# Optimization experiments

Hardware: AMD Instinct MI355X
Metric: run time of the kernel (lower is better)

Reference implementation:

```python
import jax, jax.numpy as jnp
import numpy as np

BN_EPS = 1e-5
STRIDE = 2


def setup_inputs() -> dict:
    key = jax.random.key(0)
    ks = jax.random.split(key, 8)
    B, T, Cin = 32, 1024, 128
    F, K, H = 256, 5, 512
    return {
        "x": jax.random.normal(ks[0], (B, T, Cin), jnp.float32),
        "conv_w": jax.random.normal(ks[1], (F, Cin, K), jnp.float32) * 0.05,
        "conv_b": jax.random.normal(ks[2], (F,), jnp.float32) * 0.05,
        "bn_gamma": jnp.ones((F,), jnp.float32),
        "bn_beta": jnp.zeros((F,), jnp.float32),
        "bn_mean": jnp.zeros((F,), jnp.float32),
        "bn_var": jnp.ones((F,), jnp.float32),
        "w_ih": jax.random.normal(ks[3], (4 * H, F), jnp.float32) * 0.04,
        "w_hh": jax.random.normal(ks[4], (4 * H, H), jnp.float32) * 0.04,
        "b_ih": jnp.zeros((4 * H,), jnp.float32),
        "b_hh": jnp.zeros((4 * H,), jnp.float32),
        "w_uh": jax.random.normal(ks[5], (1, H), jnp.float32) * 0.04,
        "b_uh": jnp.ones((1,), jnp.float32),
    }


def _skip_lstm(xs, w_ih, w_hh, b_ih, b_hh, w_uh, b_uh):
    # xs: [B, T', F] conv features. Skip-LSTM cell (Campos et al. Skip RNN):
    # standard LSTM + binarized state-update gate u with straight-through estimator.
    B, Tc, Fdim = xs.shape
    H = w_hh.shape[1]
    h0 = jnp.zeros((B, H), xs.dtype)
    c0 = jnp.zeros((B, H), xs.dtype)
    u0 = jnp.ones((B, 1), xs.dtype)
    # precompute input contribution to gates: [T', B, 4H]
    x_proj = jnp.einsum('btf,gf->tbg', xs, w_ih) + b_ih + b_hh

    def step(carry, xp):
        h, c, u = carry
        gates = xp + h @ w_hh.T
        i, f, g, o = jnp.split(gates, 4, axis=-1)
        c_t = jax.nn.sigmoid(f) * c + jax.nn.sigmoid(i) * jnp.tanh(g)
        h_t = jax.nn.sigmoid(o) * jnp.tanh(c_t)
        # straight-through binarization of update probability
        u_bin = u + jax.lax.stop_gradient(jnp.round(u) - u)
        c_new = u_bin * c_t + (1.0 - u_bin) * c
        h_new = u_bin * h_t + (1.0 - u_bin) * h
        du = jax.nn.sigmoid(c_new @ w_uh.T + b_uh)
        u_new = u_bin * du + (1.0 - u_bin) * (u + jnp.minimum(du, 1.0 - u))
        return (h_new, c_new, u_new), h_new

    _, hs = jax.lax.scan(step, (h0, c0, u0), x_proj)
    return jnp.swapaxes(hs, 0, 1)  # [B, T', H]


def reference(x, conv_w, conv_b, bn_gamma, bn_beta, bn_mean, bn_var,
              w_ih, w_hh, b_ih, b_hh, w_uh, b_uh):
    # Conv1d + ReLU + BatchNorm1d (eval-mode stats) on [B, Cin, T]
    xc = jnp.swapaxes(x, 1, 2)
    y = jax.lax.conv_general_dilated(
        xc, conv_w, (STRIDE,), 'VALID',
        dimension_numbers=('NCH', 'OIH', 'NCH'))
    y = jax.nn.relu(y + conv_b[None, :, None])
    inv = bn_gamma / jnp.sqrt(bn_var + BN_EPS)
    y = y * inv[None, :, None] + (bn_beta - bn_mean * inv)[None, :, None]
    y = jnp.swapaxes(y, 1, 2)  # [B, T', F]
    hs = _skip_lstm(y, w_ih, w_hh, b_ih, b_hh, w_uh, b_uh)
    return hs[:, -1, :]
```

## Files before the change

### kernel.cpp

```cpp
#include <hip/hip_runtime.h>
#include <stdint.h>
#include <math.h>

#define BB 32
#define TT 1024
#define CIN 128
#define FF 256
#define KW 5
#define HH 512
#define TP 510
#define TLAST 509
#define KC 640
#define GWG 256

#define HPK_OFF     0ull
#define PRT_OFF     262144ull
#define XP_OFF      278528ull
#define XH_OFF      (XP_OFF + 134217728ull)
#define XL_OFF      (XH_OFF + 8388608ull)
#define XSH_OFF     (XL_OFF + 8388608ull)
#define XSL_OFF     (XSH_OFF + 8388608ull)
#define WCH_OFF     (XSL_OFF + 8388608ull)
#define WCL_OFF     (WCH_OFF + 327680ull)
#define WIHH_OFF    (WCL_OFF + 327680ull)
#define WIHL_OFF    (WIHH_OFF + 1048576ull)
#define WS_NEED     (WIHL_OFF + 1048576ull)

typedef unsigned short u16;
typedef unsigned long long u64;
typedef __attribute__((ext_vector_type(8))) short short8;
typedef __attribute__((ext_vector_type(4))) float f32x4;
typedef __attribute__((ext_vector_type(4))) unsigned int u32x4;

__device__ __forceinline__ u16 f2bf(float f) {
  uint32_t u = __float_as_uint(f);
  u += 0x7fffu + ((u >> 16) & 1u);
  return (u16)(u >> 16);
}
__device__ __forceinline__ float bf2f(u16 s) { return __uint_as_float(((uint32_t)s) << 16); }
__device__ __forceinline__ void splitf(float v, u16& h, u16& l) {
  h = f2bf(v);
  l = f2bf(v - bf2f(h));
}
__device__ __forceinline__ float sigm(float x) {
  return __fdividef(1.f, 1.f + __expf(-x));
}
__device__ __forceinline__ float tanh_fast(float x) {
  float xc = fminf(x, 20.f);
  float e = __expf(2.f * xc);
  return (e - 1.f) * __fdividef(1.f, e + 1.f);
}

__global__ void prep_kernel(const float* __restrict__ x, const float* __restrict__ conv_w,
                            const float* __restrict__ w_ih,
                            u16* __restrict__ xh, u16* __restrict__ xl,
                            u16* __restrict__ wch, u16* __restrict__ wcl,
                            u16* __restrict__ wihh, u16* __restrict__ wihl) {
  int i = blockIdx.x * 256 + threadIdx.x;
  if (i < 4194304) {
    u16 h, l; splitf(x[i], h, l); xh[i] = h; xl[i] = l;
  } else if (i < 4194304 + 163840) {
    int j = i - 4194304;
    int f = j / 640, kk = j % 640;
    int c = kk & 127, k = kk >> 7;
    u16 h, l; splitf(conv_w[f * 640 + c * 5 + k], h, l);
    wch[f * 640 + kk] = h; wcl[f * 640 + kk] = l;
  } else if (i < 4194304 + 163840 + 524288) {
    int j = i - (4194304 + 163840);
    u16 h, l; splitf(w_ih[j], h, l); wihh[j] = h; wihl[j] = l;
  }
}

template <int MODE>
__global__ __launch_bounds__(256, 1) void gemm_kernel(
    const u16* __restrict__ Ah, const u16* __restrict__ Al,
    const u16* __restrict__ Bh, const u16* __restrict__ Bl,
    const float* __restrict__ e0, const float* __restrict__ e1,
    const float* __restrict__ e2, const float* __restrict__ e3, const float* __restrict__ e4,
    u16* __restrict__ outh, u16* __restrict__ outl, float* __restrict__ outf) {
  const int KDIM = (MODE == 0) ? KC : 256;
  const int MT   = (MODE == 0) ? 2 : 16;
  int bx = blockIdx.x;
  int m0 = (bx % MT) * 128;
  int n0 = (bx / MT) * 128;
  __shared__ __attribute__((aligned(16))) u16 lds[4][4096];
  int t = threadIdx.x;
  int wave = t >> 6, lane = t & 63;
  int wm = wave & 1, wn = wave >> 1;

  f32x4 acc[4][4];
#pragma unroll
  for (int i = 0; i < 4; i++)
#pragma unroll
    for (int j = 0; j < 4; j++) acc[i][j] = (f32x4){0.f, 0.f, 0.f, 0.f};

  for (int k0 = 0; k0 < KDIM; k0 += 32) {
    __syncthreads();
#pragma unroll
    for (int half = 0; half < 2; half++) {
      int e = half * 256 + t;
      int l = e & 63, tile = e >> 6;
      int kk = k0 + ((l >> 4) * 8);
      {
        int row = m0 + tile * 16 + (l & 15);
        const u16* sh = Ah + (long)row * KDIM + kk;
        const u16* sl = Al + (long)row * KDIM + kk;
        *(short8*)&lds[0][e * 8] = *(const short8*)sh;
        *(short8*)&lds[1][e * 8] = *(const short8*)sl;
      }
      {
        int n = n0 + tile * 16 + (l & 15);
        long base;
        if (MODE == 0) {
          int tp = n >> 5; if (tp > TLAST) tp = TLAST;
          base = (long)(n & 31) * 131072 + (long)tp * 256;
        } else {
          base = (long)n * 256;
        }
        *(short8*)&lds[2][e * 8] = *(const short8*)(Bh + base + kk);
        *(short8*)&lds[3][e * 8] = *(const short8*)(Bl + base + kk);
      }
    }
    __syncthreads();
    short8 af[4][2], bf[4][2];
#pragma unroll
    for (int i = 0; i < 4; i++) {
      af[i][0] = *(const short8*)&lds[0][((wm * 4 + i) * 64 + lane) * 8];
      af[i][1] = *(const short8*)&lds[1][((wm * 4 + i) * 64 + lane) * 8];
      bf[i][0] = *(const short8*)&lds[2][((wn * 4 + i) * 64 + lane) * 8];
      bf[i][1] = *(const short8*)&lds[3][((wn * 4 + i) * 64 + lane) * 8];
    }
#pragma unroll
    for (int am = 0; am < 4; am++)
#pragma unroll
      for (int an = 0; an < 4; an++) {
        acc[am][an] = __builtin_amdgcn_mfma_f32_16x16x32_bf16(af[am][0], bf[an][0], acc[am][an], 0, 0, 0);
        acc[am][an] = __builtin_amdgcn_mfma_f32_16x16x32_bf16(af[am][0], bf[an][1], acc[am][an], 0, 0, 0);
        acc[am][an] = __builtin_amdgcn_mfma_f32_16x16x32_bf16(af[am][1], bf[an][0], acc[am][an], 0, 0, 0);
      }
  }
#pragma unroll
  for (int am = 0; am < 4; am++)
#pragma unroll
    for (int an = 0; an < 4; an++) {
      int n = n0 + (wn * 4 + an) * 16 + (lane & 15);
#pragma unroll
      for (int r = 0; r < 4; r++) {
        int m = m0 + (wm * 4 + am) * 16 + (lane >> 4) * 4 + r;
        float v = acc[am][an][r];
        if (MODE == 0) {
          float inv = e1[m] / sqrtf(e4[m] + 1e-5f);
          float sh  = e2[m] - e3[m] * inv;
          v = fmaxf(v + e0[m], 0.f) * inv + sh;
          u16 h, l; splitf(v, h, l);
          outh[(long)n * 256 + m] = h;
          outl[(long)n * 256 + m] = l;
        } else {
          v += e0[m] + e1[m];
          int tp = n >> 5, b = n & 31;
          int grp = b >> 2, bb = b & 3;
          int q = m >> 9, unit = m & 511;
          int sl = unit >> 4, jjj = unit & 15;
          outf[(((long)grp * 512 + tp) * 32 + sl) * 256 + q * 64 + jjj * 4 + bb] = v;
        }
      }
    }
}

__global__ __launch_bounds__(256, 1) void scan_kernel(
    const float* __restrict__ xpg,
    const float* __restrict__ w_hh,
    const float* __restrict__ w_uh,
    const float* __restrict__ b_uh_p,
    uint32_t* __restrict__ hpk,
    u64* __restrict__ prt,
    float* __restrict__ outp)
{
  __shared__ __attribute__((aligned(16))) u16 sh_hi[4 * 528];
  __shared__ __attribute__((aligned(16))) u16 sh_lo[4 * 528];
  __shared__ float gpart[4][4][16][5];
  __shared__ float sparts[4][32];
  __shared__ int   arrive_l[32];
  __shared__ float u_l[4], ubin_l[4];
  __shared__ float wuh_l[16];
  int group = blockIdx.x & 7, slot = blockIdx.x >> 3;
  int t = threadIdx.x;
  int wave = t >> 6, lane = t & 63;
  int um = lane & 15, kq = lane >> 4;
  int nbc = um & 3;

  if (t < 16) wuh_l[t] = w_uh[slot * 16 + t];
  if (t < 4)  { u_l[t] = 1.0f; ubin_l[t] = 1.0f; }
  if (t < 32) arrive_l[t] = 0;

  short8 wfh[4][4], wfl[4][4];
#pragma unroll
  for (int q = 0; q < 4; q++) {
    long row = (long)(q * 512 + slot * 16 + um) * 512;
#pragma unroll
    for (int k4 = 0; k4 < 4; k4++) {
      union { short8 v; u16 u[8]; } Uh, Ul;
      long col0 = wave * 128 + k4 * 32 + kq * 8;
#pragma unroll
      for (int i = 0; i < 8; i++) splitf(w_hh[row + col0 + i], Uh.u[i], Ul.u[i]);
      wfh[q][k4] = Uh.v; wfl[q][k4] = Ul.v;
    }
  }
  float bu = b_uh_p[0];

  bool cell = (lane < 16);
  int  cb = wave, cj = lane;
  float c_reg = 0.f, h_reg = 0.f;

  uint32_t* hgrp = hpk + (long)group * 4096;
  u64*      pgrp = prt + (long)group * 256;

  __syncthreads();

  for (int s = 0; s < TP; s++) {
    int par = s & 1, np = par ^ 1;
    f32x4 xq;
    if (cell) {
      const float* xb = xpg + (((long)group * 512 + s) * 32 + slot) * 256;
      float x0 = xb[0 * 64 + cj * 4 + cb];
      float x1 = xb[1 * 64 + cj * 4 + cb];
      float x2 = xb[2 * 64 + cj * 4 + cb];
      float x3 = xb[3 * 64 + cj * 4 + cb];
      xq = (f32x4){x0, x1, x2, x3};
    }
    int b = t >> 6, u0 = (t & 63) * 8;
    if (s == 0) {
      *(u32x4*)&sh_hi[b * 528 + u0] = (u32x4){0u, 0u, 0u, 0u};
      *(u32x4*)&sh_lo[b * 528 + u0] = (u32x4){0u, 0u, 0u, 0u};
    } else {
      int pslot = (t & 63) >> 1;
      const u64* pw = pgrp + (long)par * 128 + b * 32 + pslot;
      const u64* hp = (const u64*)(hgrp + (long)par * 2048 + b * 512 + u0);
      uint32_t tg = (uint32_t)s;
      uint32_t e = (((uint32_t)(s - 1) >> 1) & 1u) ^ 1u;
      bool needp = ((t & 1) == 0);
      u64 v0 = __hip_atomic_load(hp,     __ATOMIC_RELAXED, __HIP_MEMORY_SCOPE_AGENT);
      u64 v1 = __hip_atomic_load(hp + 1, __ATOMIC_RELAXED, __HIP_MEMORY_SCOPE_AGENT);
      u64 v2 = __hip_atomic_load(hp + 2, __ATOMIC_RELAXED, __HIP_MEMORY_SCOPE_AGENT);
      u64 v3 = __hip_atomic_load(hp + 3, __ATOMIC_RELAXED, __HIP_MEMORY_SCOPE_AGENT);
      u64 w0 = 0;
      if (b == 0 || needp)
        w0 = __hip_atomic_load(pw, __ATOMIC_RELAXED, __HIP_MEMORY_SCOPE_AGENT);
      if (b == 0) {
        u64 w = w0;
        while ((uint32_t)(w >> 32) != tg)
          w = __hip_atomic_load(pw, __ATOMIC_RELAXED, __HIP_MEMORY_SCOPE_AGENT);
        if (needp) {
          sparts[0][pslot] = __uint_as_float((uint32_t)w);
          ((volatile int*)arrive_l)[pslot] = s;
        }
      } else {
        volatile int* arr = (volatile int*)&arrive_l[pslot];
        while (*arr != s) {}
        if (needp) {
          u64 w = w0;
          while ((uint32_t)(w >> 32) != tg)
            w = __hip_atomic_load(pw, __ATOMIC_RELAXED, __HIP_MEMORY_SCOPE_AGENT);
          sparts[b][pslot] = __uint_as_float((uint32_t)w);
        }
      }
      for (;;) {
        uint32_t bad = (((uint32_t)v0 ^ e) | ((uint32_t)(v0 >> 32) ^ e) |
                        ((uint32_t)v1 ^ e) | ((uint32_t)(v1 >> 32) ^ e) |
                        ((uint32_t)v2 ^ e) | ((uint32_t)(v2 >> 32) ^ e) |
                        ((uint32_t)v3 ^ e) | ((uint32_t)(v3 >> 32) ^ e)) & 1u;
        if (!bad) break;
        v0 = __hip_atomic_load(hp,     __ATOMIC_RELAXED, __HIP_MEMORY_SCOPE_AGENT);
        v1 = __hip_atomic_load(hp + 1, __ATOMIC_RELAXED, __HIP_MEMORY_SCOPE_AGENT);
        v2 = __hip_atomic_load(hp + 2, __ATOMIC_RELAXED, __HIP_MEMORY_SCOPE_AGENT);
        v3 = __hip_atomic_load(hp + 3, __ATOMIC_RELAXED, __HIP_MEMORY_SCOPE_AGENT);
      }
      uint32_t p[8] = {(uint32_t)v0, (uint32_t)(v0 >> 32), (uint32_t)v1, (uint32_t)(v1 >> 32),
                       (uint32_t)v2, (uint32_t)(v2 >> 32), (uint32_t)v3, (uint32_t)(v3 >> 32)};
      u32x4 hv, lv;
#pragma unroll
      for (int r = 0; r < 4; r++) {
        hv[r] = __builtin_amdgcn_perm(p[2 * r + 1], p[2 * r], 0x07060302u);
        lv[r] = __builtin_amdgcn_perm(p[2 * r + 1], p[2 * r], 0x05040100u);
      }
      *(u32x4*)&sh_hi[b * 528 + u0] = hv;
      *(u32x4*)&sh_lo[b * 528 + u0] = lv;
    }
    __syncthreads();
    if (s > 0 && t < 4) {
      float a = 0.f;
#pragma unroll
      for (int i = 0; i < 32; i++) a += sparts[t][i];
      float du = sigm(a + bu);
      float up = u_l[t], ubp = ubin_l[t];
      float un = (ubp > 0.5f) ? du : (up + fminf(du, 1.f - up));
      u_l[t] = un; ubin_l[t] = rintf(un);
    }
    f32x4 A0[4], A1[4], A2[4];
#pragma unroll
    for (int q = 0; q < 4; q++) {
      A0[q] = (f32x4){0.f, 0.f, 0.f, 0.f}; A1[q] = A0[q]; A2[q] = A0[q];
    }
#pragma unroll
    for (int k4 = 0; k4 < 4; k4++) {
      int ko = (wave * 4 + k4) * 32 + kq * 8;
      short8 bh = *(const short8*)&sh_hi[nbc * 528 + ko];
      short8 bl = *(const short8*)&sh_lo[nbc * 528 + ko];
#pragma unroll
      for (int q = 0; q < 4; q++) {
        A0[q] = __builtin_amdgcn_mfma_f32_16x16x32_bf16(wfh[q][k4], bh, A0[q], 0, 0, 0);
        A1[q] = __builtin_amdgcn_mfma_f32_16x16x32_bf16(wfh[q][k4], bl, A1[q], 0, 0, 0);
        A2[q] = __builtin_amdgcn_mfma_f32_16x16x32_bf16(wfl[q][k4], bh, A2[q], 0, 0, 0);
      }
    }
    if (um < 4) {
#pragma unroll
      for (int q = 0; q < 4; q++)
#pragma unroll
        for (int r = 0; r < 4; r++)
          gpart[wave][q][kq * 4 + r][um] = (A0[q][r] + A1[q][r]) + A2[q][r];
    }
    __syncthreads();
    if (cell) {
      float g[4];
#pragma unroll
      for (int q = 0; q < 4; q++) {
        float a = xq[q];
#pragma unroll
        for (int w = 0; w < 4; w++) a += gpart[w][q][cj][cb];
        g[q] = a;
      }
      float ig = sigm(g[0]), fg = sigm(g[1]), og = sigm(g[3]);
      float gt = tanh_fast(g[2]);
      float ct = fg * c_reg + ig * gt;
      float ht = og * tanh_fast(ct);
      bool upd = ubin_l[cb] > 0.5f;
      float cn = upd ? ct : c_reg;
      float hn = upd ? ht : h_reg;
      c_reg = cn; h_reg = hn;
      u16 hhi, hlo; splitf(hn, hhi, hlo);
      uint32_t mk = (((uint32_t)s >> 1) & 1u) ^ 1u;
      hlo = (u16)((hlo & 0xFFFEu) | mk);
      uint32_t pk = ((uint32_t)hhi << 16) | (uint32_t)hlo;
      __hip_atomic_store(hgrp + (long)np * 2048 + cb * 512 + slot * 16 + cj, pk,
                         __ATOMIC_RELAXED, __HIP_MEMORY_SCOPE_AGENT);
      float pr = cn * wuh_l[cj];
      pr += __shfl_xor(pr, 1); pr += __shfl_xor(pr, 2);
      pr += __shfl_xor(pr, 4); pr += __shfl_xor(pr, 8);
      if (s == TLAST) outp[(long)(group * 4 + cb) * 512 + slot * 16 + cj] = hn;
      if (cj == 0) {
        u64 pw = ((u64)(uint32_t)(s + 1) << 32) | (u64)__float_as_uint(pr);
        __hip_atomic_store(pgrp + (long)np * 128 + cb * 32 + slot, pw,
                           __ATOMIC_RELAXED, __HIP_MEMORY_SCOPE_AGENT);
      }
    }
  }
}

extern "C" void kernel_launch(void* const* d_in, const int* in_sizes, int n_in,
                              void* d_out, int out_size, void* d_ws, size_t ws_size,
                              hipStream_t stream) {
  const float* x      = (const float*)d_in[0];
  const float* conv_w = (const float*)d_in[1];
  const float* conv_b = (const float*)d_in[2];
  const float* gamma  = (const float*)d_in[3];
  const float* beta   = (const float*)d_in[4];
  const float* mean   = (const float*)d_in[5];
  const float* var    = (const float*)d_in[6];
  const float* w_ih   = (const float*)d_in[7];
  const float* w_hh   = (const float*)d_in[8];
  const float* b_ih   = (const float*)d_in[9];
  const float* b_hh   = (const float*)d_in[10];
  const float* w_uh   = (const float*)d_in[11];
  const float* b_uh   = (const float*)d_in[12];
  float* out = (float*)d_out;

  if (ws_size < WS_NEED) return;

  char* w = (char*)d_ws;
  uint32_t* hpk = (uint32_t*)(w + HPK_OFF);
  u64*   prt   = (u64*)(w + PRT_OFF);
  float* xp    = (float*)(w + XP_OFF);
  u16*   xh    = (u16*)(w + XH_OFF);
  u16*   xl    = (u16*)(w + XL_OFF);
  u16*   xsh   = (u16*)(w + XSH_OFF);
  u16*   xsl   = (u16*)(w + XSL_OFF);
  u16*   wch   = (u16*)(w + WCH_OFF);
  u16*   wcl   = (u16*)(w + WCL_OFF);
  u16*   wihh  = (u16*)(w + WIHH_OFF);
  u16*   wihl  = (u16*)(w + WIHL_OFF);


  prep_kernel<<<19072, 256, 0, stream>>>(x, conv_w, w_ih, xh, xl, wch, wcl, wihh, wihl);

  gemm_kernel<0><<<2 * 128, 256, 0, stream>>>(wch, wcl, xh, xl,
                                              conv_b, gamma, beta, mean, var,
                                              xsh, xsl, nullptr);
  gemm_kernel<1><<<16 * 128, 256, 0, stream>>>(wihh, wihl, xsh, xsl,
                                               b_ih, b_hh, nullptr, nullptr, nullptr,
                                               nullptr, nullptr, xp);
  scan_kernel<<<GWG, 256, 0, stream>>>(xp, w_hh, w_uh, b_uh, hpk, prt, out);
}
```

Before: 1.725 ms.

## Regroup scan into 2 groups of 16 batch rows to fill MFMA columns

The recurrent scan now splits the 32 batch rows into 2 groups of 16 instead of 8 groups of 4, cutting the workgroup count from 256 to 64. Each workgroup now fills all 16 MFMA N columns with distinct batch rows rather than replicating 4, and every lane performs a cell update. The x-projection output layout and the inter-workgroup flag and partial-sum buffers are resized to match. This removes wasted MFMA columns and idle lanes, but each step now moves more h data per workgroup and fewer CUs share the work.

```diff
diff --git a/kernel.cpp b/kernel.cpp
--- a/kernel.cpp
+++ b/kernel.cpp
@@ -11,7 +11,7 @@
 #define TP 510
 #define TLAST 509
 #define KC 640
-#define GWG 256
+#define GWG 64
 
 #define HPK_OFF     0ull
 #define PRT_OFF     262144ull
@@ -31,6 +31,8 @@
 typedef __attribute__((ext_vector_type(8))) short short8;
 typedef __attribute__((ext_vector_type(4))) float f32x4;
 typedef __attribute__((ext_vector_type(4))) unsigned int u32x4;
+
+#define AL(p) __hip_atomic_load((p), __ATOMIC_RELAXED, __HIP_MEMORY_SCOPE_AGENT)
 
 __device__ __forceinline__ u16 f2bf(float f) {
   uint32_t u = __float_as_uint(f);
@@ -158,10 +160,10 @@
         } else {
           v += e0[m] + e1[m];
           int tp = n >> 5, b = n & 31;
-          int grp = b >> 2, bb = b & 3;
+          int grp = b >> 4, bb = b & 15;
           int q = m >> 9, unit = m & 511;
           int sl = unit >> 4, jjj = unit & 15;
-          outf[(((long)grp * 512 + tp) * 32 + sl) * 256 + q * 64 + jjj * 4 + bb] = v;
+          outf[((((long)grp * 512 + tp) * 32 + sl) * 4 + q) * 256 + bb * 16 + jjj] = v;
         }
       }
     }
@@ -176,21 +178,20 @@
     u64* __restrict__ prt,
     float* __restrict__ outp)
 {
-  __shared__ __attribute__((aligned(16))) u16 sh_hi[4 * 528];
-  __shared__ __attribute__((aligned(16))) u16 sh_lo[4 * 528];
-  __shared__ float gpart[4][4][16][5];
-  __shared__ float sparts[4][32];
+  __shared__ __attribute__((aligned(16))) u16 sh_hi[16 * 528];
+  __shared__ __attribute__((aligned(16))) u16 sh_lo[16 * 528];
+  __shared__ float gpart[4][4][16][17];
+  __shared__ float sparts[16][32];
   __shared__ int   arrive_l[32];
-  __shared__ float u_l[4], ubin_l[4];
+  __shared__ float u_l[16], ubin_l[16];
   __shared__ float wuh_l[16];
-  int group = blockIdx.x & 7, slot = blockIdx.x >> 3;
+  int group = blockIdx.x & 1, slot = blockIdx.x >> 1;
   int t = threadIdx.x;
   int wave = t >> 6, lane = t & 63;
   int um = lane & 15, kq = lane >> 4;
-  int nbc = um & 3;
 
   if (t < 16) wuh_l[t] = w_uh[slot * 16 + t];
-  if (t < 4)  { u_l[t] = 1.0f; ubin_l[t] = 1.0f; }
+  if (t < 16) { u_l[t] = 1.0f; ubin_l[t] = 1.0f; }
   if (t < 32) arrive_l[t] = 0;
 
   short8 wfh[4][4], wfl[4][4];
@@ -208,86 +209,92 @@
   }
   float bu = b_uh_p[0];
 
-  bool cell = (lane < 16);
-  int  cb = wave, cj = lane;
+  int cb = wave * 4 + kq, cj = um;
   float c_reg = 0.f, h_reg = 0.f;
 
-  uint32_t* hgrp = hpk + (long)group * 4096;
-  u64*      pgrp = prt + (long)group * 256;
+  uint32_t* hgrp = hpk + (long)group * 16384;
+  u64*      pgrp = prt + (long)group * 1024;
 
   __syncthreads();
 
   for (int s = 0; s < TP; s++) {
     int par = s & 1, np = par ^ 1;
     f32x4 xq;
-    if (cell) {
-      const float* xb = xpg + (((long)group * 512 + s) * 32 + slot) * 256;
-      float x0 = xb[0 * 64 + cj * 4 + cb];
-      float x1 = xb[1 * 64 + cj * 4 + cb];
-      float x2 = xb[2 * 64 + cj * 4 + cb];
-      float x3 = xb[3 * 64 + cj * 4 + cb];
-      xq = (f32x4){x0, x1, x2, x3};
-    }
-    int b = t >> 6, u0 = (t & 63) * 8;
+    {
+      const float* xb = xpg + (((long)group * 512 + s) * 32 + slot) * 1024;
+      xq = (f32x4){xb[0 * 256 + wave * 64 + lane],
+                   xb[1 * 256 + wave * 64 + lane],
+                   xb[2 * 256 + wave * 64 + lane],
+                   xb[3 * 256 + wave * 64 + lane]};
+    }
+    int b0 = (t >> 6) * 4, u0 = (t & 63) * 8;
+    int pslot = (t & 63) >> 1;
     if (s == 0) {
-      *(u32x4*)&sh_hi[b * 528 + u0] = (u32x4){0u, 0u, 0u, 0u};
-      *(u32x4*)&sh_lo[b * 528 + u0] = (u32x4){0u, 0u, 0u, 0u};
+#pragma unroll
+      for (int bi = 0; bi < 4; bi++) {
+        *(u32x4*)&sh_hi[(b0 + bi) * 528 + u0] = (u32x4){0u, 0u, 0u, 0u};
+        *(u32x4*)&sh_lo[(b0 + bi) * 528 + u0] = (u32x4){0u, 0u, 0u, 0u};
+      }
     } else {
-      int pslot = (t & 63) >> 1;
-      const u64* pw = pgrp + (long)par * 128 + b * 32 + pslot;
-      const u64* hp = (const u64*)(hgrp + (long)par * 2048 + b * 512 + u0);
       uint32_t tg = (uint32_t)s;
       uint32_t e = (((uint32_t)(s - 1) >> 1) & 1u) ^ 1u;
-      bool needp = ((t & 1) == 0);
-      u64 v0 = __hip_atomic_load(hp,     __ATOMIC_RELAXED, __HIP_MEMORY_SCOPE_AGENT);
-      u64 v1 = __hip_atomic_load(hp + 1, __ATOMIC_RELAXED, __HIP_MEMORY_SCOPE_AGENT);
-      u64 v2 = __hip_atomic_load(hp + 2, __ATOMIC_RELAXED, __HIP_MEMORY_SCOPE_AGENT);
-      u64 v3 = __hip_atomic_load(hp + 3, __ATOMIC_RELAXED, __HIP_MEMORY_SCOPE_AGENT);
-      u64 w0 = 0;
-      if (b == 0 || needp)
-        w0 = __hip_atomic_load(pw, __ATOMIC_RELAXED, __HIP_MEMORY_SCOPE_AGENT);
-      if (b == 0) {
-        u64 w = w0;
-        while ((uint32_t)(w >> 32) != tg)
-          w = __hip_atomic_load(pw, __ATOMIC_RELAXED, __HIP_MEMORY_SCOPE_AGENT);
-        if (needp) {
-          sparts[0][pslot] = __uint_as_float((uint32_t)w);
-          ((volatile int*)arrive_l)[pslot] = s;
-        }
+      int pb1 = b0 + ((t & 1) << 1), pb2 = pb1 + 1;
+      const u64* pw1 = pgrp + (long)par * 512 + (long)pb1 * 32 + pslot;
+      const u64* pw2 = pw1 + 32;
+      u64 v[4][4];
+#pragma unroll
+      for (int bi = 0; bi < 4; bi++) {
+        const u64* hp = (const u64*)(hgrp + (long)par * 8192 + (b0 + bi) * 512 + u0);
+#pragma unroll
+        for (int k = 0; k < 4; k++) v[bi][k] = AL(hp + k);
+      }
+      u64 w1 = AL(pw1), w2 = AL(pw2);
+      if (t < 64) {
+        const u64* pd = pgrp + (long)par * 512 + pslot;
+        u64 wd = AL(pd);
+        while ((uint32_t)(wd >> 32) != tg) wd = AL(pd);
+        if ((t & 1) == 0) ((volatile int*)arrive_l)[pslot] = s;
       } else {
         volatile int* arr = (volatile int*)&arrive_l[pslot];
         while (*arr != s) {}
-        if (needp) {
-          u64 w = w0;
-          while ((uint32_t)(w >> 32) != tg)
-            w = __hip_atomic_load(pw, __ATOMIC_RELAXED, __HIP_MEMORY_SCOPE_AGENT);
-          sparts[b][pslot] = __uint_as_float((uint32_t)w);
+      }
+      while ((uint32_t)(w1 >> 32) != tg) w1 = AL(pw1);
+      sparts[pb1][pslot] = __uint_as_float((uint32_t)w1);
+      while ((uint32_t)(w2 >> 32) != tg) w2 = AL(pw2);
+      sparts[pb2][pslot] = __uint_as_float((uint32_t)w2);
+      for (;;) {
+        uint32_t bad = 0;
+#pragma unroll
+        for (int bi = 0; bi < 4; bi++)
+#pragma unroll
+          for (int k = 0; k < 4; k++)
+            bad |= ((uint32_t)v[bi][k] ^ e) | ((uint32_t)(v[bi][k] >> 32) ^ e);
+        if (!(bad & 1u)) break;
+#pragma unroll
+        for (int bi = 0; bi < 4; bi++) {
+          const u64* hp = (const u64*)(hgrp + (long)par * 8192 + (b0 + bi) * 512 + u0);
+#pragma unroll
+          for (int k = 0; k < 4; k++) v[bi][k] = AL(hp + k);
         }
       }
-      for (;;) {
-        uint32_t bad = (((uint32_t)v0 ^ e) | ((uint32_t)(v0 >> 32) ^ e) |
-                        ((uint32_t)v1 ^ e) | ((uint32_t)(v1 >> 32) ^ e) |
-                        ((uint32_t)v2 ^ e) | ((uint32_t)(v2 >> 32) ^ e) |
-                        ((uint32_t)v3 ^ e) | ((uint32_t)(v3 >> 32) ^ e)) & 1u;
-        if (!bad) break;
-        v0 = __hip_atomic_load(hp,     __ATOMIC_RELAXED, __HIP_MEMORY_SCOPE_AGENT);
-        v1 = __hip_atomic_load(hp + 1, __ATOMIC_RELAXED, __HIP_MEMORY_SCOPE_AGENT);
-        v2 = __hip_atomic_load(hp + 2, __ATOMIC_RELAXED, __HIP_MEMORY_SCOPE_AGENT);
-        v3 = __hip_atomic_load(hp + 3, __ATOMIC_RELAXED, __HIP_MEMORY_SCOPE_AGENT);
-      }
-      uint32_t p[8] = {(uint32_t)v0, (uint32_t)(v0 >> 32), (uint32_t)v1, (uint32_t)(v1 >> 32),
-                       (uint32_t)v2, (uint32_t)(v2 >> 32), (uint32_t)v3, (uint32_t)(v3 >> 32)};
-      u32x4 hv, lv;
-#pragma unroll
-      for (int r = 0; r < 4; r++) {
-        hv[r] = __builtin_amdgcn_perm(p[2 * r + 1], p[2 * r], 0x07060302u);
-        lv[r] = __builtin_amdgcn_perm(p[2 * r + 1], p[2 * r], 0x05040100u);
-      }
-      *(u32x4*)&sh_hi[b * 528 + u0] = hv;
-      *(u32x4*)&sh_lo[b * 528 + u0] = lv;
+#pragma unroll
+      for (int bi = 0; bi < 4; bi++) {
+        uint32_t p[8] = {(uint32_t)v[bi][0], (uint32_t)(v[bi][0] >> 32),
+                         (uint32_t)v[bi][1], (uint32_t)(v[bi][1] >> 32),
+                         (uint32_t)v[bi][2], (uint32_t)(v[bi][2] >> 32),
+                         (uint32_t)v[bi][3], (uint32_t)(v[bi][3] >> 32)};
+        u32x4 hv, lv;
+#pragma unroll
+        for (int r = 0; r < 4; r++) {
+          hv[r] = __builtin_amdgcn_perm(p[2 * r + 1], p[2 * r], 0x07060302u);
+          lv[r] = __builtin_amdgcn_perm(p[2 * r + 1], p[2 * r], 0x05040100u);
+        }
+        *(u32x4*)&sh_hi[(b0 + bi) * 528 + u0] = hv;
+        *(u32x4*)&sh_lo[(b0 + bi) * 528 + u0] = lv;
+      }
     }
     __syncthreads();
-    if (s > 0 && t < 4) {
+    if (s > 0 && t < 16) {
       float a = 0.f;
 #pragma unroll
       for (int i = 0; i < 32; i++) a += sparts[t][i];
@@ -304,8 +311,8 @@
 #pragma unroll
     for (int k4 = 0; k4 < 4; k4++) {
       int ko = (wave * 4 + k4) * 32 + kq * 8;
-      short8 bh = *(const short8*)&sh_hi[nbc * 528 + ko];
-      short8 bl = *(const short8*)&sh_lo[nbc * 528 + ko];
+      short8 bh = *(const short8*)&sh_hi[um * 528 + ko];
+      short8 bl = *(const short8*)&sh_lo[um * 528 + ko];
 #pragma unroll
       for (int q = 0; q < 4; q++) {
         A0[q] = __builtin_amdgcn_mfma_f32_16x16x32_bf16(wfh[q][k4], bh, A0[q], 0, 0, 0);
@@ -313,7 +320,7 @@
         A2[q] = __builtin_amdgcn_mfma_f32_16x16x32_bf16(wfl[q][k4], bh, A2[q], 0, 0, 0);
       }
     }
-    if (um < 4) {
+    {
 #pragma unroll
       for (int q = 0; q < 4; q++)
 #pragma unroll
@@ -321,7 +328,7 @@
           gpart[wave][q][kq * 4 + r][um] = (A0[q][r] + A1[q][r]) + A2[q][r];
     }
     __syncthreads();
-    if (cell) {
+    {
       float g[4];
 #pragma unroll
       for (int q = 0; q < 4; q++) {
@@ -342,15 +349,15 @@
       uint32_t mk = (((uint32_t)s >> 1) & 1u) ^ 1u;
       hlo = (u16)((hlo & 0xFFFEu) | mk);
       uint32_t pk = ((uint32_t)hhi << 16) | (uint32_t)hlo;
-      __hip_atomic_store(hgrp + (long)np * 2048 + cb * 512 + slot * 16 + cj, pk,
+      __hip_atomic_store(hgrp + (long)np * 8192 + cb * 512 + slot * 16 + cj, pk,
                          __ATOMIC_RELAXED, __HIP_MEMORY_SCOPE_AGENT);
       float pr = cn * wuh_l[cj];
       pr += __shfl_xor(pr, 1); pr += __shfl_xor(pr, 2);
       pr += __shfl_xor(pr, 4); pr += __shfl_xor(pr, 8);
-      if (s == TLAST) outp[(long)(group * 4 + cb) * 512 + slot * 16 + cj] = hn;
+      if (s == TLAST) outp[(long)(group * 16 + cb) * 512 + slot * 16 + cj] = hn;
       if (cj == 0) {
-        u64 pw = ((u64)(uint32_t)(s + 1) << 32) | (u64)__float_as_uint(pr);
-        __hip_atomic_store(pgrp + (long)np * 128 + cb * 32 + slot, pw,
+        u64 pwv = ((u64)(uint32_t)(s + 1) << 32) | (u64)__float_as_uint(pr);
+        __hip_atomic_store(pgrp + (long)np * 512 + cb * 32 + slot, pwv,
                            __ATOMIC_RELAXED, __HIP_MEMORY_SCOPE_AGENT);
       }
     }
```

New measurement: 2.003 ms. 1.16x slower.
